# Kernel tuning notes

Hardware: AMD Instinct MI355X
Metric: run time of the kernel (lower is better)

## Reference

```python
import jax, jax.numpy as jnp
import numpy as np
import math

SR = 44100  # sampling_rate from init_kwargs


def setup_inputs() -> dict:
    key = jax.random.key(0)
    k1, k2, k3, k4 = jax.random.split(key, 4)
    B, T, C = 32, 262144, 1024
    x = jax.random.normal(k1, (B, T), jnp.float32)
    # rescale uniform [0,1) to realistic formant parameter ranges
    freq = jax.random.uniform(k2, (B, C), jnp.float32) * 3800.0 + 200.0  # Hz
    bw = jax.random.uniform(k3, (B, C), jnp.float32) * 400.0 + 50.0      # Hz
    gain = jax.random.uniform(k4, (B, C), jnp.float32) + 0.1
    return {"x": x, "freq": freq, "bw": bw, "gain": gain}


def _coeffs(freq, bw, gain, T):
    """Vectorized per-sample biquad coefficients via linear interpolation of controls."""
    nyquist = SR / 2
    fn = jnp.clip(freq / nyquist, 1e-5, 0.95)  # [B, C]
    bn = jnp.clip(bw / nyquist, 1e-5, 0.95)
    C = freq.shape[1]
    t = jnp.arange(T, dtype=jnp.float32)
    cf = t / (T / C)                      # control-rate fractional index per sample
    idx = jnp.floor(cf).astype(jnp.int32)
    frac = cf - idx                       # [T]
    nxt = jnp.minimum(idx + 1, C - 1)

    def interp(v):  # [B,C] -> [B,T]
        return v[:, idx] * (1.0 - frac) + v[:, nxt] * frac

    f_t = interp(fn)
    b_t = interp(bn)
    g_t = interp(gain)
    omega = (2.0 * math.pi) * f_t
    sin_w = jnp.sin(omega)
    cos_w = jnp.cos(omega)
    alpha = sin_w * jnp.sinh((math.log(2.0) / 2.0) * b_t * omega / sin_w)
    a0 = 1.0 + alpha
    b0 = alpha * g_t / a0
    b2 = -alpha * g_t / a0   # b1 == 0, term dropped
    a1 = -2.0 * cos_w / a0
    a2 = (1.0 - alpha) / a0
    return b0, b2, a1, a2    # each [B, T]


def reference(x, freq, bw, gain):
    B, T = x.shape
    b0, b2, a1, a2 = _coeffs(freq, bw, gain, T)

    def step(carry, inp):
        y1, y2, x1, x2 = carry
        xt, b0t, b2t, a1t, a2t = inp
        y = b0t * xt + b2t * x2 - a1t * y1 - a2t * y2
        return (y, y1, xt, x1), y

    z = jnp.zeros((B,), x.dtype)
    seq = (x.T, b0.T, b2.T, a1.T, a2.T)  # each [T, B]
    (y1, y2, x1, x2), ys = jax.lax.scan(step, (z, z, z, z), seq)
    return ys.T, (y1, y2, x1, x2)
```

## Files before the change

kernel.cpp:

```cpp
#include <hip/hip_runtime.h>
#include <hip/hip_bf16.h>

#define BB 32
#define TT 262144
#define CC 1024
#define LL 32
#define THREADS 256
#define BLKROW 32
#define NBLK (BB*BLKROW)
#define NT (NBLK*THREADS)
#define SPB (THREADS*LL)
#define PIDX(l) ((((l)>>5)*33) + ((l)&31))

typedef float f32x4 __attribute__((ext_vector_type(4)));

__device__ __forceinline__ float clipn(float v){
  return fminf(fmaxf(v, 1e-5f), 0.95f);
}

__device__ __forceinline__ void coef(float fn, float bn, float gt,
                                     float& b0c, float& p1, float& p2){
  float cw = __builtin_amdgcn_cosf(fn);
  float alpha = 2.1775860903036022f * bn * fn;
  float inv = __builtin_amdgcn_rcpf(1.0f + alpha);
  b0c = alpha*gt*inv;
  p1  = 2.0f*cw*inv;
  p2  = (alpha - 1.0f)*inv;
}

__device__ __forceinline__ void ctrl(const float* __restrict__ fqp,
                                     const float* __restrict__ bwp,
                                     const float* __restrict__ gnp,
                                     int b, int t0,
                                     float& f0, float& df, float& w0, float& dw,
                                     float& g0, float& dg, float& fr0){
  int idx = t0 >> 8;
  int nx  = idx + 1 < CC ? idx + 1 : CC - 1;
  const float inyq = 1.0f/22050.0f;
  int cb = b*CC;
  f0 = clipn(fqp[cb+idx]*inyq);
  float f1 = clipn(fqp[cb+nx]*inyq);
  w0 = clipn(bwp[cb+idx]*inyq);
  float w1 = clipn(bwp[cb+nx]*inyq);
  g0 = gnp[cb+idx];
  float g1 = gnp[cb+nx];
  df = f1-f0; dw = w1-w0; dg = g1-g0;
  fr0 = (float)(t0 & 255) * (1.0f/256.0f);
}

__device__ __forceinline__ void segMapReg(const float* xr, float xs2, float xs1,
                                          float f0,float df,float w0,float dw,
                                          float g0,float dg,float fr0,
                                          float& m00,float& m01,float& m10,float& m11,
                                          float& v0,float& v1){
  m00=1.f;m01=0.f;m10=0.f;m11=1.f;v0=0.f;v1=0.f;
  float xm2 = xs2, xm1 = xs1;
#pragma unroll
  for (int j=0;j<LL;++j){
    float frac = fr0 + (float)j*(1.0f/256.0f);
    float b0c,p1,p2;
    coef(f0+df*frac, w0+dw*frac, g0+dg*frac, b0c, p1, p2);
    float xc = xr[j];
    float w = b0c*(xc - xm2);
    float n00 = p1*m00 + p2*m10;
    float n01 = p1*m01 + p2*m11;
    float nv0 = p1*v0 + p2*v1 + w;
    m10=m00; m11=m01; m00=n00; m01=n01;
    v1=v0; v0=nv0;
    xm2=xm1; xm1=xc;
  }
}

__device__ __forceinline__ void waveScan(int lane,
    float& m00,float& m01,float& m10,float& m11,float& v0,float& v1){
#pragma unroll
  for (int d=1; d<64; d<<=1){
    float p00=__shfl_up(m00,(unsigned)d,64), p01=__shfl_up(m01,(unsigned)d,64),
          p10=__shfl_up(m10,(unsigned)d,64), p11=__shfl_up(m11,(unsigned)d,64),
          pv0=__shfl_up(v0,(unsigned)d,64),  pv1=__shfl_up(v1,(unsigned)d,64);
    if (lane >= d){
      float n00=m00*p00+m01*p10, n01=m00*p01+m01*p11;
      float n10=m10*p00+m11*p10, n11=m10*p01+m11*p11;
      float nv0=m00*pv0+m01*pv1+v0, nv1=m10*pv0+m11*pv1+v1;
      m00=n00;m01=n01;m10=n10;m11=n11;v0=nv0;v1=nv1;
    }
  }
}

__device__ __forceinline__ void stageIn(const float* __restrict__ src, float* tile, int tid){
  const float4* s4 = reinterpret_cast<const float4*>(src);
#pragma unroll
  for (int k=0;k<8;++k){
    float4 v = s4[tid + k*256];
    int p = PIDX((tid + k*256)*4);
    tile[p]=v.x; tile[p+1]=v.y; tile[p+2]=v.z; tile[p+3]=v.w;
  }
}

__global__ __launch_bounds__(THREADS) void mapScan(
    const float* __restrict__ x, const float* __restrict__ fqp,
    const float* __restrict__ bwp, const float* __restrict__ gnp,
    float* __restrict__ ws){
  __shared__ float wagg[4][6];
  const int blkId = blockIdx.x;
  const int row = blkId >> 5;
  const int blk = blkId & 31;
  const int tid = threadIdx.x;
  const int lane = tid & 63;
  const int wid = tid >> 6;
  const int g = blkId*THREADS + tid;
  const int t0 = blk*SPB + tid*LL;
  const float* xb = x + (size_t)row*TT;

  float xr[LL];
  {
    const float4* xv = reinterpret_cast<const float4*>(xb + t0);
#pragma unroll
    for (int q=0;q<LL/4;++q){
      float4 v = xv[q];
      xr[4*q]=v.x; xr[4*q+1]=v.y; xr[4*q+2]=v.z; xr[4*q+3]=v.w;
    }
  }
  float xs1 = __shfl_up(xr[31], 1u, 64);
  float xs2 = __shfl_up(xr[30], 1u, 64);
  if (lane == 0){
    if (t0 > 0){ xs1 = xb[t0-1]; xs2 = xb[t0-2]; }
    else       { xs1 = 0.f;      xs2 = 0.f; }
  }

  float f0,df,w0,dw,g0,dg,fr0;
  ctrl(fqp,bwp,gnp,row,t0,f0,df,w0,dw,g0,dg,fr0);

  float m00,m01,m10,m11,v0,v1;
  segMapReg(xr, xs2, xs1, f0,df,w0,dw,g0,dg,fr0, m00,m01,m10,m11,v0,v1);

  waveScan(lane, m00,m01,m10,m11,v0,v1);
  if (lane == 63){
    wagg[wid][0]=m00; wagg[wid][1]=m01; wagg[wid][2]=m10;
    wagg[wid][3]=m11; wagg[wid][4]=v0;  wagg[wid][5]=v1;
  }
  float e00=__shfl_up(m00,1u,64), e01=__shfl_up(m01,1u,64),
        e10=__shfl_up(m10,1u,64), e11=__shfl_up(m11,1u,64),
        ev0=__shfl_up(v0,1u,64),  ev1=__shfl_up(v1,1u,64);
  if (lane == 0){ e00=1.f;e01=0.f;e10=0.f;e11=1.f;ev0=0.f;ev1=0.f; }
  __syncthreads();

  float W00=1.f,W01=0.f,W10=0.f,W11=1.f,Wv0=0.f,Wv1=0.f;
  for (int w=0; w<wid; ++w){
    float A0=wagg[w][0],A1=wagg[w][1],A2=wagg[w][2],
          A3=wagg[w][3],A4=wagg[w][4],A5=wagg[w][5];
    float n00=A0*W00+A1*W10, n01=A0*W01+A1*W11;
    float n10=A2*W00+A3*W10, n11=A2*W01+A3*W11;
    float nv0=A0*Wv0+A1*Wv1+A4, nv1=A2*Wv0+A3*Wv1+A5;
    W00=n00;W01=n01;W10=n10;W11=n11;Wv0=nv0;Wv1=nv1;
  }
  float F00 = e00*W00 + e01*W10, F01 = e00*W01 + e01*W11;
  float F10 = e10*W00 + e11*W10, F11 = e10*W01 + e11*W11;
  float Fv0 = e00*Wv0 + e01*Wv1 + ev0;
  float Fv1 = e10*Wv0 + e11*Wv1 + ev1;

  float2* fw = reinterpret_cast<float2*>(ws);
  fw[0*NT + g] = make_float2(F00, F01);
  fw[1*NT + g] = make_float2(F10, F11);
  fw[2*NT + g] = make_float2(Fv0, Fv1);

  if (tid == 0){
    float B00=1.f,B01=0.f,B10=0.f,B11=1.f,Bv0=0.f,Bv1=0.f;
#pragma unroll
    for (int w=0; w<4; ++w){
      float A0=wagg[w][0],A1=wagg[w][1],A2=wagg[w][2],
            A3=wagg[w][3],A4=wagg[w][4],A5=wagg[w][5];
      float n00=A0*B00+A1*B10, n01=A0*B01+A1*B11;
      float n10=A2*B00+A3*B10, n11=A2*B01+A3*B11;
      float nv0=A0*Bv0+A1*Bv1+A4, nv1=A2*Bv0+A3*Bv1+A5;
      B00=n00;B01=n01;B10=n10;B11=n11;Bv0=nv0;Bv1=nv1;
    }
    float* aggf = ws + (size_t)6*NT + blkId*6;
    aggf[0]=B00; aggf[1]=B01; aggf[2]=B10; aggf[3]=B11; aggf[4]=Bv0; aggf[5]=Bv1;
  }
}

__global__ __launch_bounds__(THREADS) void replay(
    const float* __restrict__ x, const float* __restrict__ fqp,
    const float* __restrict__ bwp, const float* __restrict__ gnp,
    const float* __restrict__ ws, float* __restrict__ out){
  __shared__ float tile[THREADS*33];
  __shared__ float svb[2];
  const int blkId = blockIdx.x;
  const int row = blkId >> 5;
  const int blk = blkId & 31;
  const int tid = threadIdx.x;
  const int g = blkId*THREADS + tid;
  const int t0 = blk*SPB + tid*LL;
  const float* xb = x + (size_t)row*TT;

  const float2* fw = reinterpret_cast<const float2*>(ws);
  float2 q0 = fw[0*NT + g];
  float2 q1 = fw[1*NT + g];
  float2 q2 = fw[2*NT + g];

  stageIn(xb + blk*SPB, tile, tid);

  float f0,df,w0,dw,g0,dg,fr0;
  ctrl(fqp,bwp,gnp,row,t0,f0,df,w0,dw,g0,dg,fr0);

  float F00=q0.x, F01=q0.y, F10=q1.x, F11=q1.y, Fv0=q2.x, Fv1=q2.y;

  if (tid < 32){
    const float* aggf = ws + (size_t)6*NT + (row*32 + tid)*6;
    float A0=aggf[0],A1=aggf[1],A2=aggf[2],A3=aggf[3],A4=aggf[4],A5=aggf[5];
#pragma unroll
    for (int d=1; d<32; d<<=1){
      float p00=__shfl_up(A0,(unsigned)d,32), p01=__shfl_up(A1,(unsigned)d,32),
            p10=__shfl_up(A2,(unsigned)d,32), p11=__shfl_up(A3,(unsigned)d,32),
            pv0=__shfl_up(A4,(unsigned)d,32), pv1=__shfl_up(A5,(unsigned)d,32);
      if (tid >= d){
        float n00=A0*p00+A1*p10, n01=A0*p01+A1*p11;
        float n10=A2*p00+A3*p10, n11=A2*p01+A3*p11;
        float nv0=A0*pv0+A1*pv1+A4, nv1=A2*pv0+A3*pv1+A5;
        A0=n00;A1=n01;A2=n10;A3=n11;A4=nv0;A5=nv1;
      }
    }
    float pv0 = 0.f, pv1 = 0.f;
    if (blk > 0){
      pv0 = __shfl(A4, blk-1, 32);
      pv1 = __shfl(A5, blk-1, 32);
    }
    if (tid==0){ svb[0]=pv0; svb[1]=pv1; }
  }
  __syncthreads();

  float xs1, xs2;
  if (tid > 0){
    xs1 = tile[(tid-1)*33 + 31];
    xs2 = tile[(tid-1)*33 + 30];
  } else if (blk > 0){
    xs1 = xb[blk*SPB - 1];
    xs2 = xb[blk*SPB - 2];
  } else { xs1 = 0.f; xs2 = 0.f; }

  float bv0 = svb[0], bv1 = svb[1];
  float y1 = F00*bv0 + F01*bv1 + Fv0;
  float y2 = F10*bv0 + F11*bv1 + Fv1;

  float* xrow = tile + tid*33;
  float xm2 = xs2, xm1 = xs1;
#pragma unroll
  for (int j=0;j<LL;++j){
    float frac = fr0 + (float)j*(1.0f/256.0f);
    float b0c,p1,p2;
    coef(f0+df*frac, w0+dw*frac, g0+dg*frac, b0c, p1, p2);
    float xc = xrow[j];
    float y = b0c*(xc - xm2) + p1*y1 + p2*y2;
    xrow[j] = y;
    y2=y1; y1=y;
    xm2=xm1; xm1=xc;
  }
  __syncthreads();

  float* ob = out + (size_t)row*TT + blk*SPB;
  f32x4* o4 = reinterpret_cast<f32x4*>(ob);
#pragma unroll
  for (int k=0;k<8;++k){
    int p = PIDX((tid + k*256)*4);
    f32x4 v = { tile[p], tile[p+1], tile[p+2], tile[p+3] };
    __builtin_nontemporal_store(v, &o4[tid + k*256]);
  }
  if (blk==31 && tid==THREADS-1){
    size_t base = (size_t)BB*TT;
    out[base + row]        = y1;
    out[base + BB + row]   = y2;
    out[base + 2*BB + row] = xm1;
    out[base + 3*BB + row] = xm2;
  }
}

extern "C" void kernel_launch(void* const* d_in, const int* in_sizes, int n_in,
                              void* d_out, int out_size, void* d_ws, size_t ws_size,
                              hipStream_t stream) {
  const float* x  = (const float*)d_in[0];
  const float* fq = (const float*)d_in[1];
  const float* bw = (const float*)d_in[2];
  const float* gn = (const float*)d_in[3];
  float* out = (float*)d_out;
  float* ws  = (float*)d_ws;

  hipLaunchKernelGGL(mapScan, dim3(NBLK), dim3(THREADS), 0, stream, x, fq, bw, gn, ws);
  hipLaunchKernelGGL(replay,  dim3(NBLK), dim3(THREADS), 0, stream, x, fq, bw, gn, ws, out);
}
```

Baseline: 29.82 us.

## Halve per-thread segment length and store scan prefixes in fp16

Halves the samples per thread, which doubles the block count per row to 64 and widens the cross-block prefix scan to a full 64-lane wave. It also stores the per-thread prefix transforms in the workspace as fp16 pairs instead of fp32. Both changes target workspace traffic and per-thread serial latency. The fp16 storage of the 2x2 transfer matrices and offset vectors loses precision, which can raise output error. The shorter segments also mean more blocks and more scan overhead.

```diff
diff --git a/kernel.cpp b/kernel.cpp
--- a/kernel.cpp
+++ b/kernel.cpp
@@ -1,18 +1,20 @@
 #include <hip/hip_runtime.h>
 #include <hip/hip_bf16.h>
+#include <hip/hip_fp16.h>
 
 #define BB 32
 #define TT 262144
 #define CC 1024
-#define LL 32
+#define LL 16
 #define THREADS 256
-#define BLKROW 32
+#define BLKROW 64
 #define NBLK (BB*BLKROW)
 #define NT (NBLK*THREADS)
 #define SPB (THREADS*LL)
 #define PIDX(l) ((((l)>>5)*33) + ((l)&31))
 
-typedef float f32x4 __attribute__((ext_vector_type(4)));
+typedef float    f32x4 __attribute__((ext_vector_type(4)));
+typedef _Float16 f16x2 __attribute__((ext_vector_type(2)));
 
 __device__ __forceinline__ float clipn(float v){
   return fminf(fmaxf(v, 1e-5f), 0.95f);
@@ -90,7 +92,7 @@
 __device__ __forceinline__ void stageIn(const float* __restrict__ src, float* tile, int tid){
   const float4* s4 = reinterpret_cast<const float4*>(src);
 #pragma unroll
-  for (int k=0;k<8;++k){
+  for (int k=0;k<4;++k){
     float4 v = s4[tid + k*256];
     int p = PIDX((tid + k*256)*4);
     tile[p]=v.x; tile[p+1]=v.y; tile[p+2]=v.z; tile[p+3]=v.w;
@@ -100,11 +102,11 @@
 __global__ __launch_bounds__(THREADS) void mapScan(
     const float* __restrict__ x, const float* __restrict__ fqp,
     const float* __restrict__ bwp, const float* __restrict__ gnp,
-    float* __restrict__ ws){
+    void* __restrict__ ws){
   __shared__ float wagg[4][6];
   const int blkId = blockIdx.x;
-  const int row = blkId >> 5;
-  const int blk = blkId & 31;
+  const int row = blkId >> 6;
+  const int blk = blkId & 63;
   const int tid = threadIdx.x;
   const int lane = tid & 63;
   const int wid = tid >> 6;
@@ -121,8 +123,8 @@
       xr[4*q]=v.x; xr[4*q+1]=v.y; xr[4*q+2]=v.z; xr[4*q+3]=v.w;
     }
   }
-  float xs1 = __shfl_up(xr[31], 1u, 64);
-  float xs2 = __shfl_up(xr[30], 1u, 64);
+  float xs1 = __shfl_up(xr[LL-1], 1u, 64);
+  float xs2 = __shfl_up(xr[LL-2], 1u, 64);
   if (lane == 0){
     if (t0 > 0){ xs1 = xb[t0-1]; xs2 = xb[t0-2]; }
     else       { xs1 = 0.f;      xs2 = 0.f; }
@@ -159,10 +161,13 @@
   float Fv0 = e00*Wv0 + e01*Wv1 + ev0;
   float Fv1 = e10*Wv0 + e11*Wv1 + ev1;
 
-  float2* fw = reinterpret_cast<float2*>(ws);
-  fw[0*NT + g] = make_float2(F00, F01);
-  fw[1*NT + g] = make_float2(F10, F11);
-  fw[2*NT + g] = make_float2(Fv0, Fv1);
+  f16x2* fw = reinterpret_cast<f16x2*>(ws);
+  f16x2 h0 = { (_Float16)F00, (_Float16)F01 };
+  f16x2 h1 = { (_Float16)F10, (_Float16)F11 };
+  f16x2 h2 = { (_Float16)Fv0, (_Float16)Fv1 };
+  fw[0*NT + g] = h0;
+  fw[1*NT + g] = h1;
+  fw[2*NT + g] = h2;
 
   if (tid == 0){
     float B00=1.f,B01=0.f,B10=0.f,B11=1.f,Bv0=0.f,Bv1=0.f;
@@ -175,7 +180,7 @@
       float nv0=A0*Bv0+A1*Bv1+A4, nv1=A2*Bv0+A3*Bv1+A5;
       B00=n00;B01=n01;B10=n10;B11=n11;Bv0=nv0;Bv1=nv1;
     }
-    float* aggf = ws + (size_t)6*NT + blkId*6;
+    float* aggf = (float*)((char*)ws + (size_t)NT*12) + blkId*6;
     aggf[0]=B00; aggf[1]=B01; aggf[2]=B10; aggf[3]=B11; aggf[4]=Bv0; aggf[5]=Bv1;
   }
 }
@@ -183,37 +188,39 @@
 __global__ __launch_bounds__(THREADS) void replay(
     const float* __restrict__ x, const float* __restrict__ fqp,
     const float* __restrict__ bwp, const float* __restrict__ gnp,
-    const float* __restrict__ ws, float* __restrict__ out){
-  __shared__ float tile[THREADS*33];
+    const void* __restrict__ ws, float* __restrict__ out){
+  __shared__ float tile[(THREADS*LL/32)*33];
   __shared__ float svb[2];
   const int blkId = blockIdx.x;
-  const int row = blkId >> 5;
-  const int blk = blkId & 31;
+  const int row = blkId >> 6;
+  const int blk = blkId & 63;
   const int tid = threadIdx.x;
   const int g = blkId*THREADS + tid;
   const int t0 = blk*SPB + tid*LL;
   const float* xb = x + (size_t)row*TT;
 
-  const float2* fw = reinterpret_cast<const float2*>(ws);
-  float2 q0 = fw[0*NT + g];
-  float2 q1 = fw[1*NT + g];
-  float2 q2 = fw[2*NT + g];
+  const f16x2* fw = reinterpret_cast<const f16x2*>(ws);
+  f16x2 h0 = fw[0*NT + g];
+  f16x2 h1 = fw[1*NT + g];
+  f16x2 h2 = fw[2*NT + g];
 
   stageIn(xb + blk*SPB, tile, tid);
 
   float f0,df,w0,dw,g0,dg,fr0;
   ctrl(fqp,bwp,gnp,row,t0,f0,df,w0,dw,g0,dg,fr0);
 
-  float F00=q0.x, F01=q0.y, F10=q1.x, F11=q1.y, Fv0=q2.x, Fv1=q2.y;
-
-  if (tid < 32){
-    const float* aggf = ws + (size_t)6*NT + (row*32 + tid)*6;
+  float F00=(float)h0.x, F01=(float)h0.y;
+  float F10=(float)h1.x, F11=(float)h1.y;
+  float Fv0=(float)h2.x, Fv1=(float)h2.y;
+
+  if (tid < 64){
+    const float* aggf = (const float*)((const char*)ws + (size_t)NT*12) + (row*64 + tid)*6;
     float A0=aggf[0],A1=aggf[1],A2=aggf[2],A3=aggf[3],A4=aggf[4],A5=aggf[5];
 #pragma unroll
-    for (int d=1; d<32; d<<=1){
-      float p00=__shfl_up(A0,(unsigned)d,32), p01=__shfl_up(A1,(unsigned)d,32),
-            p10=__shfl_up(A2,(unsigned)d,32), p11=__shfl_up(A3,(unsigned)d,32),
-            pv0=__shfl_up(A4,(unsigned)d,32), pv1=__shfl_up(A5,(unsigned)d,32);
+    for (int d=1; d<64; d<<=1){
+      float p00=__shfl_up(A0,(unsigned)d,64), p01=__shfl_up(A1,(unsigned)d,64),
+            p10=__shfl_up(A2,(unsigned)d,64), p11=__shfl_up(A3,(unsigned)d,64),
+            pv0=__shfl_up(A4,(unsigned)d,64), pv1=__shfl_up(A5,(unsigned)d,64);
       if (tid >= d){
         float n00=A0*p00+A1*p10, n01=A0*p01+A1*p11;
         float n10=A2*p00+A3*p10, n11=A2*p01+A3*p11;
@@ -223,8 +230,8 @@
     }
     float pv0 = 0.f, pv1 = 0.f;
     if (blk > 0){
-      pv0 = __shfl(A4, blk-1, 32);
-      pv1 = __shfl(A5, blk-1, 32);
+      pv0 = __shfl(A4, blk-1, 64);
+      pv1 = __shfl(A5, blk-1, 64);
     }
     if (tid==0){ svb[0]=pv0; svb[1]=pv1; }
   }
@@ -232,8 +239,8 @@
 
   float xs1, xs2;
   if (tid > 0){
-    xs1 = tile[(tid-1)*33 + 31];
-    xs2 = tile[(tid-1)*33 + 30];
+    xs1 = tile[PIDX(tid*LL - 1)];
+    xs2 = tile[PIDX(tid*LL - 2)];
   } else if (blk > 0){
     xs1 = xb[blk*SPB - 1];
     xs2 = xb[blk*SPB - 2];
@@ -243,16 +250,16 @@
   float y1 = F00*bv0 + F01*bv1 + Fv0;
   float y2 = F10*bv0 + F11*bv1 + Fv1;
 
-  float* xrow = tile + tid*33;
   float xm2 = xs2, xm1 = xs1;
 #pragma unroll
   for (int j=0;j<LL;++j){
     float frac = fr0 + (float)j*(1.0f/256.0f);
     float b0c,p1,p2;
     coef(f0+df*frac, w0+dw*frac, g0+dg*frac, b0c, p1, p2);
-    float xc = xrow[j];
+    int p = PIDX(tid*LL + j);
+    float xc = tile[p];
     float y = b0c*(xc - xm2) + p1*y1 + p2*y2;
-    xrow[j] = y;
+    tile[p] = y;
     y2=y1; y1=y;
     xm2=xm1; xm1=xc;
   }
@@ -261,12 +268,12 @@
   float* ob = out + (size_t)row*TT + blk*SPB;
   f32x4* o4 = reinterpret_cast<f32x4*>(ob);
 #pragma unroll
-  for (int k=0;k<8;++k){
+  for (int k=0;k<4;++k){
     int p = PIDX((tid + k*256)*4);
     f32x4 v = { tile[p], tile[p+1], tile[p+2], tile[p+3] };
     __builtin_nontemporal_store(v, &o4[tid + k*256]);
   }
-  if (blk==31 && tid==THREADS-1){
+  if (blk==BLKROW-1 && tid==THREADS-1){
     size_t base = (size_t)BB*TT;
     out[base + row]        = y1;
     out[base + BB + row]   = y2;
@@ -283,8 +290,7 @@
   const float* bw = (const float*)d_in[2];
   const float* gn = (const float*)d_in[3];
   float* out = (float*)d_out;
-  float* ws  = (float*)d_ws;
-
-  hipLaunchKernelGGL(mapScan, dim3(NBLK), dim3(THREADS), 0, stream, x, fq, bw, gn, ws);
-  hipLaunchKernelGGL(replay,  dim3(NBLK), dim3(THREADS), 0, stream, x, fq, bw, gn, ws, out);
-}
+
+  hipLaunchKernelGGL(mapScan, dim3(NBLK), dim3(THREADS), 0, stream, x, fq, bw, gn, d_ws);
+  hipLaunchKernelGGL(replay,  dim3(NBLK), dim3(THREADS), 0, stream, x, fq, bw, gn, d_ws, out);
+}
```

Result: slower. 32.53 us (+9.1%).
